# Kernel optimization log

Hardware: AMD Instinct MI355X
Metric: run time of the kernel (lower is better)

Reference implementation:

```python
import jax, jax.numpy as jnp
import numpy as np

N_NODES = 50000
N_EDGES = 800000
IN_DIM, HID_DIM, OUT_DIM = 128, 256, 40


def setup_inputs() -> dict:
    key = jax.random.key(0)
    ks = jax.random.split(key, 8)
    x = jax.random.normal(ks[0], (N_NODES, IN_DIM), dtype=jnp.float32)
    edge_index = jax.random.randint(ks[1], (2, N_EDGES), 0, N_NODES, dtype=jnp.int64)
    s1 = 1.0 / np.sqrt(IN_DIM)
    s2 = 1.0 / np.sqrt(HID_DIM)
    return {
        "x": x,
        "edge_index": edge_index,
        "W1_l": jax.random.normal(ks[2], (IN_DIM, HID_DIM), dtype=jnp.float32) * s1,
        "W1_r": jax.random.normal(ks[3], (IN_DIM, HID_DIM), dtype=jnp.float32) * s1,
        "b1": jnp.zeros((HID_DIM,), dtype=jnp.float32),
        "W2_l": jax.random.normal(ks[4], (HID_DIM, OUT_DIM), dtype=jnp.float32) * s2,
        "W2_r": jax.random.normal(ks[5], (HID_DIM, OUT_DIM), dtype=jnp.float32) * s2,
        "b2": jnp.zeros((OUT_DIM,), dtype=jnp.float32),
    }


def _sage_conv(x, src, dst, W_l, W_r, b, n_nodes):
    # mean aggregation of source features onto destination nodes
    agg = jax.ops.segment_sum(x[src], dst, num_segments=n_nodes)  # [N, d]
    cnt = jax.ops.segment_sum(jnp.ones(src.shape[0], x.dtype), dst, num_segments=n_nodes)
    agg = agg / jnp.maximum(cnt, 1.0)[:, None]
    # PyG SAGEConv: lin_l(aggr) + lin_r(x), bias in lin_l
    return agg @ W_l + x @ W_r + b


def reference(x, edge_index, W1_l, W1_r, b1, W2_l, W2_r, b2):
    src, dst = edge_index[0], edge_index[1]
    n = x.shape[0]
    h = jax.nn.relu(_sage_conv(x, src, dst, W1_l, W1_r, b1, n))
    # dropout is identity in eval mode
    out = _sage_conv(h, src, dst, W2_l, W2_r, b2, n)
    return jax.nn.log_softmax(out, axis=1)
```

## Files before the change

### kernel.cpp

```cpp
#include <hip/hip_runtime.h>
#include <hip/hip_bf16.h>

#define N_NODES 50000
#define N_EDGES 800000
#define IN_DIM 128
#define HID_DIM 256
#define OUT_DIM 40
#define M_PAD 50048
#define NBUCKETS 782
#define EPB 8192
#define BINA_BLOCKS 98
#define BLK_PAD 128

#define OFF_RP     0
#define OFF_ESRC   200064
#define OFF_STAGE  3400064
#define OFF_HISTG  6600064
#define OFF_PFXG   7000448
#define OFF_BTOT   7400832
#define OFF_BBASE  7403968
#define OFF_AB     7407104
#define OFF_H      33031680
#define OFF_W1T    58656256
#define OFF_W2T    58787328
#define OFF_P2     58828288
#define OFF_R2     62832128

typedef __attribute__((ext_vector_type(8))) short short8;
typedef __attribute__((ext_vector_type(4))) float f32x4;

__device__ __forceinline__ float bfu2f(unsigned u) {
  union { unsigned i; float f; } c; c.i = u << 16; return c.f;
}
__device__ __forceinline__ unsigned f2bfu(float f) {
  union { float f; unsigned i; } c; c.f = f;
  return (c.i + 0x7fffu + ((c.i >> 16) & 1u)) >> 16;
}

#define GLOAD_LDS16(g, l)                                                      \
  __builtin_amdgcn_global_load_lds(                                            \
      (const __attribute__((address_space(1))) void*)(g),                      \
      (__attribute__((address_space(3))) void*)(l), 16, 0, 0)

__global__ __launch_bounds__(1024) void k_hist(const int* __restrict__ dst,
                                               int* __restrict__ hist_g) {
  __shared__ int hist[NBUCKETS];
  int t = threadIdx.x, blk = blockIdx.x;
  for (int b = t; b < NBUCKETS; b += 1024) hist[b] = 0;
  __syncthreads();
  int e0 = blk * EPB, e1 = min(e0 + EPB, N_EDGES);
  for (int e = e0 + t; e < e1; e += 1024) atomicAdd(&hist[dst[e] >> 6], 1);
  __syncthreads();
  for (int b = t; b < NBUCKETS; b += 1024) hist_g[b * BLK_PAD + blk] = hist[b];
}

__global__ __launch_bounds__(256) void k_hscanA(const int* __restrict__ hist_g,
                                                int* __restrict__ pfx_g,
                                                int* __restrict__ btot) {
  int wave = blockIdx.x * 4 + (threadIdx.x >> 6);
  int lane = threadIdx.x & 63;
  if (wave >= NBUCKETS) return;
  const int* h = hist_g + wave * BLK_PAD;
  int v0 = (lane < BINA_BLOCKS) ? h[lane] : 0;
  int v1 = (lane + 64 < BINA_BLOCKS) ? h[lane + 64] : 0;
  int s0 = v0;
#pragma unroll
  for (int d = 1; d < 64; d <<= 1) {
    int u = __shfl_up(s0, d, 64);
    if (lane >= d) s0 += u;
  }
  int tot0 = __shfl(s0, 63, 64);
  int s1 = v1;
#pragma unroll
  for (int d = 1; d < 64; d <<= 1) {
    int u = __shfl_up(s1, d, 64);
    if (lane >= d) s1 += u;
  }
  s1 += tot0;
  pfx_g[wave * BLK_PAD + lane] = s0 - v0;
  if (lane + 64 < BLK_PAD) pfx_g[wave * BLK_PAD + lane + 64] = s1 - v1;
  if (lane == 63) btot[wave] = s1;
}

__global__ __launch_bounds__(1024) void k_hscanB(const int* __restrict__ btot,
                                                 int* __restrict__ bbase,
                                                 int* __restrict__ row_ptr) {
  __shared__ int part[1024];
  int t = threadIdx.x;
  int v = (t < NBUCKETS) ? btot[t] : 0;
  part[t] = v;
  __syncthreads();
  for (int off = 1; off < 1024; off <<= 1) {
    int u = (t >= off) ? part[t - off] : 0;
    __syncthreads();
    part[t] += u;
    __syncthreads();
  }
  if (t < NBUCKETS) bbase[t] = part[t] - v;
  if (t == NBUCKETS - 1) {
    bbase[NBUCKETS] = part[t];
    row_ptr[N_NODES] = part[t];
  }
}

__global__ __launch_bounds__(1024) void k_fill2(const int* __restrict__ src,
                                                const int* __restrict__ dst,
                                                const int* __restrict__ bbase,
                                                const int* __restrict__ pfx_g,
                                                unsigned* __restrict__ stage) {
  __shared__ int cur[NBUCKETS];
  int t = threadIdx.x, blk = blockIdx.x;
  for (int b = t; b < NBUCKETS; b += 1024)
    cur[b] = bbase[b] + pfx_g[b * BLK_PAD + blk];
  __syncthreads();
  int e0 = blk * EPB, e1 = min(e0 + EPB, N_EDGES);
  for (int e = e0 + t; e < e1; e += 1024) {
    int d = dst[e];
    int pos = atomicAdd(&cur[d >> 6], 1);
    stage[pos] = ((unsigned)src[e] << 6) | (unsigned)(d & 63);
  }
}

__global__ __launch_bounds__(256) void k_bsort(const unsigned* __restrict__ stage,
                                               const int* __restrict__ bbase,
                                               int* __restrict__ row_ptr,
                                               int* __restrict__ esrc) {
  __shared__ int lcnt[64];
  __shared__ int lout[1536];
  int b = blockIdx.x, t = threadIdx.x;
  int base = bbase[b];
  int nb = bbase[b + 1] - base;
  if (t < 64) lcnt[t] = 0;
  __syncthreads();
  const unsigned* sp = stage + base;
  for (int e = t; e < nb; e += 256) atomicAdd(&lcnt[sp[e] & 63u], 1);
  __syncthreads();
  if (t < 64) {
    int v = lcnt[t];
    int s = v;
#pragma unroll
    for (int d = 1; d < 64; d <<= 1) {
      int u = __shfl_up(s, d, 64);
      if (t >= d) s += u;
    }
    int node = b * 64 + t;
    if (node < N_NODES) row_ptr[node] = base + s - v;
    lcnt[t] = s - v;
  }
  __syncthreads();
  for (int e = t; e < nb; e += 256) {
    unsigned p = sp[e];
    int lp = atomicAdd(&lcnt[p & 63u], 1);
    lout[lp] = (int)(p >> 6);
  }
  __syncthreads();
  for (int i = t; i < nb; i += 256) esrc[base + i] = lout[i];
}

__global__ __launch_bounds__(256) void k_convx(const float* __restrict__ x,
                                               char* __restrict__ ABb) {
  int t = blockIdx.x * 256 + threadIdx.x;
  int row = t >> 4, c8 = (t & 15) << 3;
  if (row >= N_NODES) return;
  const float* xp = x + (size_t)row * IN_DIM + c8;
  unsigned short o[8];
#pragma unroll
  for (int i = 0; i < 8; ++i) o[i] = (unsigned short)f2bfu(xp[i]);
  *(short8*)(ABb + (size_t)row * 512 + 256 + c8 * 2) = *(short8*)o;
}

__global__ __launch_bounds__(256) void k_convw(const float* __restrict__ W1l,
                                               const float* __restrict__ W1r,
                                               const float* __restrict__ W2l,
                                               const float* __restrict__ W2r,
                                               unsigned short* __restrict__ Wt1,
                                               unsigned short* __restrict__ Wt2) {
  int k = threadIdx.x;
  if (blockIdx.x < 256) {
    int n = blockIdx.x;
    float v = (k < 128) ? W1l[(size_t)k * HID_DIM + n]
                        : W1r[(size_t)(k - 128) * HID_DIM + n];
    Wt1[(size_t)n * 256 + k] = (unsigned short)f2bfu(v);
  } else {
    int n = blockIdx.x - 256;
    float v = (n < OUT_DIM) ? W2l[(size_t)k * OUT_DIM + n]
                            : W2r[(size_t)k * OUT_DIM + (n - OUT_DIM)];
    Wt2[(size_t)n * 256 + k] = (unsigned short)f2bfu(v);
  }
}

__global__ __launch_bounds__(256) void k_agg1(char* __restrict__ ABb,
    const int* __restrict__ row_ptr, const int* __restrict__ esrc) {
  int tid = threadIdx.x;
  int node = blockIdx.x * 4 + (tid >> 6);
  int lane = tid & 63;
  int g = lane >> 4;
  int q = lane & 15;
  int beg = row_ptr[node], end = row_ptr[node + 1];
  float s[8];
#pragma unroll
  for (int j = 0; j < 8; ++j) s[j] = 0.f;

  for (int e0 = beg; e0 < end; e0 += 4) {
    int e = e0 + g;
    if (e < end) {
      int srcn = esrc[e];
      short8 v = *(const short8*)(ABb + (size_t)srcn * 512 + 256 + q * 16);
#pragma unroll
      for (int j = 0; j < 8; ++j)
        s[j] += bfu2f((unsigned short)v[j]);
    }
  }
#pragma unroll
  for (int j = 0; j < 8; ++j) {
    s[j] += __shfl_xor(s[j], 16, 64);
    s[j] += __shfl_xor(s[j], 32, 64);
  }
  float inv = 1.0f / (float)max(end - beg, 1);
  if (lane < 16) {
    unsigned short o[8];
#pragma unroll
    for (int j = 0; j < 8; ++j) o[j] = (unsigned short)f2bfu(s[j] * inv);
    *(short8*)(ABb + (size_t)node * 512 + q * 16) = *(short8*)o;
  }
}

__global__ __launch_bounds__(256) void k_gemm1(
    const char* __restrict__ ABb, const short* __restrict__ Wt1,
    const float* __restrict__ b1, unsigned short* __restrict__ H) {
  __shared__ __align__(16) char As[64 * 512];
  const int tid = threadIdx.x;
  const int w = tid >> 6, lane = tid & 63;
  const int row0 = blockIdx.x * 64;

  {
    const char* gbase = ABb + (size_t)row0 * 512;
#pragma unroll
    for (int i = 0; i < 8; ++i) {
      int o = i * 4096 + w * 1024 + lane * 16;
      int row = o >> 9;
      int kslot = ((o & 511) >> 4) ^ (row & 7);
      GLOAD_LDS16(gbase + row * 512 + kslot * 16, As + i * 4096 + w * 1024);
    }
  }
  __syncthreads();

  f32x4 acc[4][4];
#pragma unroll
  for (int mi = 0; mi < 4; ++mi)
#pragma unroll
    for (int ni = 0; ni < 4; ++ni) acc[mi][ni] = (f32x4){0.f, 0.f, 0.f, 0.f};

  const short* wb = Wt1 + (size_t)(w * 64 + (lane & 15)) * 256 + (lane >> 4) * 8;

  for (int ks = 0; ks < 8; ++ks) {
    short8 af[4], bf[4];
#pragma unroll
    for (int mi = 0; mi < 4; ++mi) {
      int row = mi * 16 + (lane & 15);
      int kslot = (ks * 4 + (lane >> 4)) ^ (row & 7);
      af[mi] = *(const short8*)(As + row * 512 + kslot * 16);
    }
#pragma unroll
    for (int ni = 0; ni < 4; ++ni)
      bf[ni] = *(const short8*)(wb + ni * 16 * 256 + ks * 32);
#pragma unroll
    for (int mi = 0; mi < 4; ++mi)
#pragma unroll
      for (int ni = 0; ni < 4; ++ni)
        acc[mi][ni] = __builtin_amdgcn_mfma_f32_16x16x32_bf16(
            af[mi], bf[ni], acc[mi][ni], 0, 0, 0);
  }

#pragma unroll
  for (int ni = 0; ni < 4; ++ni) {
    int col = w * 64 + ni * 16 + (lane & 15);
    float bv = b1[col];
#pragma unroll
    for (int mi = 0; mi < 4; ++mi) {
      int rbase = row0 + mi * 16 + (lane >> 4) * 4;
#pragma unroll
      for (int r = 0; r < 4; ++r) {
        float v = fmaxf(acc[mi][ni][r] + bv, 0.f);
        H[(size_t)(rbase + r) * 256 + col] = (unsigned short)f2bfu(v);
      }
    }
  }
}

__global__ __launch_bounds__(256) void k_gemm2(
    const char* __restrict__ Hb, const short* __restrict__ Wt2,
    const float* __restrict__ b2, unsigned short* __restrict__ P2,
    float* __restrict__ R2) {
  __shared__ __align__(16) char As[64 * 512];
  const int tid = threadIdx.x;
  const int w = tid >> 6, lane = tid & 63;
  const int row0 = blockIdx.x * 64;

  {
    const char* gbase = Hb + (size_t)row0 * 512;
#pragma unroll
    for (int i = 0; i < 8; ++i) {
      int o = i * 4096 + w * 1024 + lane * 16;
      int row = o >> 9;
      int kslot = ((o & 511) >> 4) ^ (row & 7);
      GLOAD_LDS16(gbase + row * 512 + kslot * 16, As + i * 4096 + w * 1024);
    }
  }
  __syncthreads();

  f32x4 acc[5];
#pragma unroll
  for (int ni = 0; ni < 5; ++ni) acc[ni] = (f32x4){0.f, 0.f, 0.f, 0.f};

  const short* wb = Wt2 + (size_t)(lane & 15) * 256 + (lane >> 4) * 8;
  const int arow = w * 16 + (lane & 15);

  for (int ks = 0; ks < 8; ++ks) {
    int kslot = (ks * 4 + (lane >> 4)) ^ (arow & 7);
    short8 a = *(const short8*)(As + arow * 512 + kslot * 16);
#pragma unroll
    for (int ni = 0; ni < 5; ++ni) {
      short8 bf = *(const short8*)(wb + ni * 16 * 256 + ks * 32);
      acc[ni] = __builtin_amdgcn_mfma_f32_16x16x32_bf16(a, bf, acc[ni], 0, 0, 0);
    }
  }

#pragma unroll
  for (int ni = 0; ni < 5; ++ni) {
    int col = ni * 16 + (lane & 15);
#pragma unroll
    for (int r = 0; r < 4; ++r) {
      int row = row0 + w * 16 + (lane >> 4) * 4 + r;
      float v = acc[ni][r];
      if (col < OUT_DIM) {
        P2[(size_t)row * OUT_DIM + col] = (unsigned short)f2bfu(v);
      } else {
        R2[(size_t)row * OUT_DIM + (col - OUT_DIM)] = v + b2[col - OUT_DIM];
      }
    }
  }
}

__global__ __launch_bounds__(256) void k_agg2(const unsigned short* __restrict__ P2,
    const float* __restrict__ R2, const int* __restrict__ row_ptr,
    const int* __restrict__ esrc, float* __restrict__ out) {
  int tid = threadIdx.x;
  int node = blockIdx.x * 4 + (tid >> 6);
  int lane = tid & 63;
  int g = lane >> 3;
  int q = lane & 7;
  int beg = row_ptr[node], end = row_ptr[node + 1];
  float s[8];
#pragma unroll
  for (int j = 0; j < 8; ++j) s[j] = 0.f;

  for (int e0 = beg; e0 < end; e0 += 8) {
    int e = e0 + g;
    if (e < end && q < 5) {
      int srcn = esrc[e];
      short8 v = *(const short8*)((const char*)P2 + (size_t)srcn * 80 + q * 16);
#pragma unroll
      for (int j = 0; j < 8; ++j)
        s[j] += bfu2f((unsigned short)v[j]);
    }
  }
#pragma unroll
  for (int j = 0; j < 8; ++j) {
    s[j] += __shfl_xor(s[j], 8, 64);
    s[j] += __shfl_xor(s[j], 16, 64);
    s[j] += __shfl_xor(s[j], 32, 64);
  }

  float inv = 1.0f / (float)max(end - beg, 1);
  float v[8];
  float m = -1e30f;
  if (q < 5) {
    const float* rr = R2 + (size_t)node * OUT_DIM + q * 8;
    f32x4 r0 = *(const f32x4*)rr;
    f32x4 r1 = *(const f32x4*)(rr + 4);
#pragma unroll
    for (int j = 0; j < 8; ++j) {
      float rj = (j < 4) ? r0[j] : r1[j - 4];
      v[j] = s[j] * inv + rj;
      m = fmaxf(m, v[j]);
    }
  }
#pragma unroll
  for (int o = 1; o <= 4; o <<= 1) m = fmaxf(m, __shfl_xor(m, o, 64));
  float ex = 0.f;
  if (q < 5) {
#pragma unroll
    for (int j = 0; j < 8; ++j) ex += __expf(v[j] - m);
  }
#pragma unroll
  for (int o = 1; o <= 4; o <<= 1) ex += __shfl_xor(ex, o, 64);
  float ls = __logf(ex) + m;

  if (g == 0 && q < 5) {
    float* op = out + (size_t)node * OUT_DIM + q * 8;
    f32x4 o0, o1;
#pragma unroll
    for (int j = 0; j < 4; ++j) { o0[j] = v[j] - ls; o1[j] = v[j + 4] - ls; }
    *(f32x4*)op = o0;
    *(f32x4*)(op + 4) = o1;
  }
}

extern "C" void kernel_launch(void* const* d_in, const int* in_sizes, int n_in,
                              void* d_out, int out_size, void* d_ws, size_t ws_size,
                              hipStream_t stream) {
  const float* x   = (const float*)d_in[0];
  const int*   ei  = (const int*)d_in[1];
  const float* W1l = (const float*)d_in[2];
  const float* W1r = (const float*)d_in[3];
  const float* b1  = (const float*)d_in[4];
  const float* W2l = (const float*)d_in[5];
  const float* W2r = (const float*)d_in[6];
  const float* b2  = (const float*)d_in[7];
  float* out = (float*)d_out;

  const int* src = ei;
  const int* dst = ei + N_EDGES;

  char* ws = (char*)d_ws;
  int*      row_ptr = (int*)(ws + OFF_RP);
  int*      esrc    = (int*)(ws + OFF_ESRC);
  unsigned* stage   = (unsigned*)(ws + OFF_STAGE);
  int*      hist_g  = (int*)(ws + OFF_HISTG);
  int*      pfx_g   = (int*)(ws + OFF_PFXG);
  int*      btot    = (int*)(ws + OFF_BTOT);
  int*      bbase   = (int*)(ws + OFF_BBASE);
  char*     ABb     = ws + OFF_AB;
  char*     Hb      = ws + OFF_H;
  unsigned short* Wt1 = (unsigned short*)(ws + OFF_W1T);
  unsigned short* Wt2 = (unsigned short*)(ws + OFF_W2T);
  unsigned short* P2  = (unsigned short*)(ws + OFF_P2);
  float* R2 = (float*)(ws + OFF_R2);

  (void)hipMemsetAsync(ABb + (size_t)N_NODES * 512, 0, (M_PAD - N_NODES) * 512,
                       stream);

  k_convx<<<(N_NODES * 16 + 255) / 256, 256, 0, stream>>>(x, ABb);
  k_convw<<<336, 256, 0, stream>>>(W1l, W1r, W2l, W2r, Wt1, Wt2);

  k_hist<<<BINA_BLOCKS, 1024, 0, stream>>>(dst, hist_g);
  k_hscanA<<<(NBUCKETS + 3) / 4, 256, 0, stream>>>(hist_g, pfx_g, btot);
  k_hscanB<<<1, 1024, 0, stream>>>(btot, bbase, row_ptr);
  k_fill2<<<BINA_BLOCKS, 1024, 0, stream>>>(src, dst, bbase, pfx_g, stage);
  k_bsort<<<NBUCKETS, 256, 0, stream>>>(stage, bbase, row_ptr, esrc);

  k_agg1<<<N_NODES / 4, 256, 0, stream>>>(ABb, row_ptr, esrc);
  k_gemm1<<<M_PAD / 64, 256, 0, stream>>>(ABb, (const short*)Wt1, b1,
                                          (unsigned short*)Hb);
  k_gemm2<<<M_PAD / 64, 256, 0, stream>>>(Hb, (const short*)Wt2, b2, P2, R2);
  k_agg2<<<N_NODES / 4, 256, 0, stream>>>(P2, R2, row_ptr, esrc, out);
}
```

Measured before the change: 229.0 us.

## Fuse two GEMMs through LDS, merge conversion kernels, unroll agg1 gathers

The layer-1 GEMM and the layer-2 projection GEMM now run in one kernel. The ReLU'd hidden tile is written as bf16 into the swizzled LDS buffer and consumed directly by the second MFMA loop, so the 25MB H intermediate no longer makes a round trip through global memory. The x and weight conversion kernels are merged into a single launch. agg1 now issues two neighbor gathers per iteration with clamped indices and zero weights, which raises memory-level parallelism at the cost of some redundant loads on the tail.

```diff
diff --git a/kernel.cpp b/kernel.cpp
--- a/kernel.cpp
+++ b/kernel.cpp
@@ -11,6 +11,7 @@
 #define EPB 8192
 #define BINA_BLOCKS 98
 #define BLK_PAD 128
+#define CONVX_BLOCKS 3125
 
 #define OFF_RP     0
 #define OFF_ESRC   200064
@@ -20,11 +21,10 @@
 #define OFF_BTOT   7400832
 #define OFF_BBASE  7403968
 #define OFF_AB     7407104
-#define OFF_H      33031680
-#define OFF_W1T    58656256
-#define OFF_W2T    58787328
-#define OFF_P2     58828288
-#define OFF_R2     62832128
+#define OFF_W1T    33031680
+#define OFF_W2T    33162752
+#define OFF_P2     33203712
+#define OFF_R2     37207552
 
 typedef __attribute__((ext_vector_type(8))) short short8;
 typedef __attribute__((ext_vector_type(4))) float f32x4;
@@ -157,32 +157,31 @@
   for (int i = t; i < nb; i += 256) esrc[base + i] = lout[i];
 }
 
-__global__ __launch_bounds__(256) void k_convx(const float* __restrict__ x,
-                                               char* __restrict__ ABb) {
-  int t = blockIdx.x * 256 + threadIdx.x;
-  int row = t >> 4, c8 = (t & 15) << 3;
-  if (row >= N_NODES) return;
-  const float* xp = x + (size_t)row * IN_DIM + c8;
-  unsigned short o[8];
-#pragma unroll
-  for (int i = 0; i < 8; ++i) o[i] = (unsigned short)f2bfu(xp[i]);
-  *(short8*)(ABb + (size_t)row * 512 + 256 + c8 * 2) = *(short8*)o;
-}
-
-__global__ __launch_bounds__(256) void k_convw(const float* __restrict__ W1l,
-                                               const float* __restrict__ W1r,
-                                               const float* __restrict__ W2l,
-                                               const float* __restrict__ W2r,
-                                               unsigned short* __restrict__ Wt1,
-                                               unsigned short* __restrict__ Wt2) {
-  int k = threadIdx.x;
-  if (blockIdx.x < 256) {
-    int n = blockIdx.x;
+__global__ __launch_bounds__(256) void k_conv(const float* __restrict__ x,
+                                              char* __restrict__ ABb,
+                                              const float* __restrict__ W1l,
+                                              const float* __restrict__ W1r,
+                                              const float* __restrict__ W2l,
+                                              const float* __restrict__ W2r,
+                                              unsigned short* __restrict__ Wt1,
+                                              unsigned short* __restrict__ Wt2) {
+  if (blockIdx.x < CONVX_BLOCKS) {
+    int t = blockIdx.x * 256 + threadIdx.x;
+    int row = t >> 4, c8 = (t & 15) << 3;
+    const float* xp = x + (size_t)row * IN_DIM + c8;
+    unsigned short o[8];
+#pragma unroll
+    for (int i = 0; i < 8; ++i) o[i] = (unsigned short)f2bfu(xp[i]);
+    *(short8*)(ABb + (size_t)row * 512 + 256 + c8 * 2) = *(short8*)o;
+  } else if (blockIdx.x < CONVX_BLOCKS + 256) {
+    int n = blockIdx.x - CONVX_BLOCKS;
+    int k = threadIdx.x;
     float v = (k < 128) ? W1l[(size_t)k * HID_DIM + n]
                         : W1r[(size_t)(k - 128) * HID_DIM + n];
     Wt1[(size_t)n * 256 + k] = (unsigned short)f2bfu(v);
   } else {
-    int n = blockIdx.x - 256;
+    int n = blockIdx.x - CONVX_BLOCKS - 256;
+    int k = threadIdx.x;
     float v = (n < OUT_DIM) ? W2l[(size_t)k * OUT_DIM + n]
                             : W2r[(size_t)k * OUT_DIM + (n - OUT_DIM)];
     Wt2[(size_t)n * 256 + k] = (unsigned short)f2bfu(v);
@@ -201,15 +200,22 @@
 #pragma unroll
   for (int j = 0; j < 8; ++j) s[j] = 0.f;
 
-  for (int e0 = beg; e0 < end; e0 += 4) {
-    int e = e0 + g;
-    if (e < end) {
-      int srcn = esrc[e];
-      short8 v = *(const short8*)(ABb + (size_t)srcn * 512 + 256 + q * 16);
-#pragma unroll
-      for (int j = 0; j < 8; ++j)
-        s[j] += bfu2f((unsigned short)v[j]);
-    }
+  for (int e0 = beg; e0 < end; e0 += 8) {
+    int eA = e0 + g;
+    int eB = eA + 4;
+    int iA = min(eA, end - 1);
+    int iB = min(eB, end - 1);
+    int sA = esrc[iA], sB = esrc[iB];
+    float wA = (eA < end) ? 1.f : 0.f;
+    float wB = (eB < end) ? 1.f : 0.f;
+    short8 vA = *(const short8*)(ABb + (size_t)sA * 512 + 256 + q * 16);
+    short8 vB = *(const short8*)(ABb + (size_t)sB * 512 + 256 + q * 16);
+#pragma unroll
+    for (int j = 0; j < 8; ++j)
+      s[j] = fmaf(wA, bfu2f((unsigned short)vA[j]), s[j]);
+#pragma unroll
+    for (int j = 0; j < 8; ++j)
+      s[j] = fmaf(wB, bfu2f((unsigned short)vB[j]), s[j]);
   }
 #pragma unroll
   for (int j = 0; j < 8; ++j) {
@@ -225,71 +231,9 @@
   }
 }
 
-__global__ __launch_bounds__(256) void k_gemm1(
+__global__ __launch_bounds__(256) void k_gemm(
     const char* __restrict__ ABb, const short* __restrict__ Wt1,
-    const float* __restrict__ b1, unsigned short* __restrict__ H) {
-  __shared__ __align__(16) char As[64 * 512];
-  const int tid = threadIdx.x;
-  const int w = tid >> 6, lane = tid & 63;
-  const int row0 = blockIdx.x * 64;
-
-  {
-    const char* gbase = ABb + (size_t)row0 * 512;
-#pragma unroll
-    for (int i = 0; i < 8; ++i) {
-      int o = i * 4096 + w * 1024 + lane * 16;
-      int row = o >> 9;
-      int kslot = ((o & 511) >> 4) ^ (row & 7);
-      GLOAD_LDS16(gbase + row * 512 + kslot * 16, As + i * 4096 + w * 1024);
-    }
-  }
-  __syncthreads();
-
-  f32x4 acc[4][4];
-#pragma unroll
-  for (int mi = 0; mi < 4; ++mi)
-#pragma unroll
-    for (int ni = 0; ni < 4; ++ni) acc[mi][ni] = (f32x4){0.f, 0.f, 0.f, 0.f};
-
-  const short* wb = Wt1 + (size_t)(w * 64 + (lane & 15)) * 256 + (lane >> 4) * 8;
-
-  for (int ks = 0; ks < 8; ++ks) {
-    short8 af[4], bf[4];
-#pragma unroll
-    for (int mi = 0; mi < 4; ++mi) {
-      int row = mi * 16 + (lane & 15);
-      int kslot = (ks * 4 + (lane >> 4)) ^ (row & 7);
-      af[mi] = *(const short8*)(As + row * 512 + kslot * 16);
-    }
-#pragma unroll
-    for (int ni = 0; ni < 4; ++ni)
-      bf[ni] = *(const short8*)(wb + ni * 16 * 256 + ks * 32);
-#pragma unroll
-    for (int mi = 0; mi < 4; ++mi)
-#pragma unroll
-      for (int ni = 0; ni < 4; ++ni)
-        acc[mi][ni] = __builtin_amdgcn_mfma_f32_16x16x32_bf16(
-            af[mi], bf[ni], acc[mi][ni], 0, 0, 0);
-  }
-
-#pragma unroll
-  for (int ni = 0; ni < 4; ++ni) {
-    int col = w * 64 + ni * 16 + (lane & 15);
-    float bv = b1[col];
-#pragma unroll
-    for (int mi = 0; mi < 4; ++mi) {
-      int rbase = row0 + mi * 16 + (lane >> 4) * 4;
-#pragma unroll
-      for (int r = 0; r < 4; ++r) {
-        float v = fmaxf(acc[mi][ni][r] + bv, 0.f);
-        H[(size_t)(rbase + r) * 256 + col] = (unsigned short)f2bfu(v);
-      }
-    }
-  }
-}
-
-__global__ __launch_bounds__(256) void k_gemm2(
-    const char* __restrict__ Hb, const short* __restrict__ Wt2,
+    const short* __restrict__ Wt2, const float* __restrict__ b1,
     const float* __restrict__ b2, unsigned short* __restrict__ P2,
     float* __restrict__ R2) {
   __shared__ __align__(16) char As[64 * 512];
@@ -298,7 +242,7 @@
   const int row0 = blockIdx.x * 64;
 
   {
-    const char* gbase = Hb + (size_t)row0 * 512;
+    const char* gbase = ABb + (size_t)row0 * 512;
 #pragma unroll
     for (int i = 0; i < 8; ++i) {
       int o = i * 4096 + w * 1024 + lane * 16;
@@ -309,11 +253,58 @@
   }
   __syncthreads();
 
-  f32x4 acc[5];
-#pragma unroll
-  for (int ni = 0; ni < 5; ++ni) acc[ni] = (f32x4){0.f, 0.f, 0.f, 0.f};
-
-  const short* wb = Wt2 + (size_t)(lane & 15) * 256 + (lane >> 4) * 8;
+  f32x4 acc[4][4];
+#pragma unroll
+  for (int mi = 0; mi < 4; ++mi)
+#pragma unroll
+    for (int ni = 0; ni < 4; ++ni) acc[mi][ni] = (f32x4){0.f, 0.f, 0.f, 0.f};
+
+  const short* wb1 = Wt1 + (size_t)(w * 64 + (lane & 15)) * 256 + (lane >> 4) * 8;
+
+  for (int ks = 0; ks < 8; ++ks) {
+    short8 af[4], bf[4];
+#pragma unroll
+    for (int mi = 0; mi < 4; ++mi) {
+      int row = mi * 16 + (lane & 15);
+      int kslot = (ks * 4 + (lane >> 4)) ^ (row & 7);
+      af[mi] = *(const short8*)(As + row * 512 + kslot * 16);
+    }
+#pragma unroll
+    for (int ni = 0; ni < 4; ++ni)
+      bf[ni] = *(const short8*)(wb1 + ni * 16 * 256 + ks * 32);
+#pragma unroll
+    for (int mi = 0; mi < 4; ++mi)
+#pragma unroll
+      for (int ni = 0; ni < 4; ++ni)
+        acc[mi][ni] = __builtin_amdgcn_mfma_f32_16x16x32_bf16(
+            af[mi], bf[ni], acc[mi][ni], 0, 0, 0);
+  }
+
+  __syncthreads();
+
+#pragma unroll
+  for (int ni = 0; ni < 4; ++ni) {
+    int col = w * 64 + ni * 16 + (lane & 15);
+    float bv = b1[col];
+#pragma unroll
+    for (int mi = 0; mi < 4; ++mi) {
+#pragma unroll
+      for (int r = 0; r < 4; ++r) {
+        int row = mi * 16 + (lane >> 4) * 4 + r;
+        float v = fmaxf(acc[mi][ni][r] + bv, 0.f);
+        int gr = (col >> 3) ^ (row & 7);
+        *(unsigned short*)(As + row * 512 + gr * 16 + (col & 7) * 2) =
+            (unsigned short)f2bfu(v);
+      }
+    }
+  }
+  __syncthreads();
+
+  f32x4 acc2[5];
+#pragma unroll
+  for (int ni = 0; ni < 5; ++ni) acc2[ni] = (f32x4){0.f, 0.f, 0.f, 0.f};
+
+  const short* wb2 = Wt2 + (size_t)(lane & 15) * 256 + (lane >> 4) * 8;
   const int arow = w * 16 + (lane & 15);
 
   for (int ks = 0; ks < 8; ++ks) {
@@ -321,8 +312,8 @@
     short8 a = *(const short8*)(As + arow * 512 + kslot * 16);
 #pragma unroll
     for (int ni = 0; ni < 5; ++ni) {
-      short8 bf = *(const short8*)(wb + ni * 16 * 256 + ks * 32);
-      acc[ni] = __builtin_amdgcn_mfma_f32_16x16x32_bf16(a, bf, acc[ni], 0, 0, 0);
+      short8 bf = *(const short8*)(wb2 + ni * 16 * 256 + ks * 32);
+      acc2[ni] = __builtin_amdgcn_mfma_f32_16x16x32_bf16(a, bf, acc2[ni], 0, 0, 0);
     }
   }
 
@@ -332,7 +323,7 @@
 #pragma unroll
     for (int r = 0; r < 4; ++r) {
       int row = row0 + w * 16 + (lane >> 4) * 4 + r;
-      float v = acc[ni][r];
+      float v = acc2[ni][r];
       if (col < OUT_DIM) {
         P2[(size_t)row * OUT_DIM + col] = (unsigned short)f2bfu(v);
       } else {
@@ -432,7 +423,6 @@
   int*      btot    = (int*)(ws + OFF_BTOT);
   int*      bbase   = (int*)(ws + OFF_BBASE);
   char*     ABb     = ws + OFF_AB;
-  char*     Hb      = ws + OFF_H;
   unsigned short* Wt1 = (unsigned short*)(ws + OFF_W1T);
   unsigned short* Wt2 = (unsigned short*)(ws + OFF_W2T);
   unsigned short* P2  = (unsigned short*)(ws + OFF_P2);
@@ -441,8 +431,8 @@
   (void)hipMemsetAsync(ABb + (size_t)N_NODES * 512, 0, (M_PAD - N_NODES) * 512,
                        stream);
 
-  k_convx<<<(N_NODES * 16 + 255) / 256, 256, 0, stream>>>(x, ABb);
-  k_convw<<<336, 256, 0, stream>>>(W1l, W1r, W2l, W2r, Wt1, Wt2);
+  k_conv<<<CONVX_BLOCKS + 336, 256, 0, stream>>>(x, ABb, W1l, W1r, W2l, W2r,
+                                                 Wt1, Wt2);
 
   k_hist<<<BINA_BLOCKS, 1024, 0, stream>>>(dst, hist_g);
   k_hscanA<<<(NBUCKETS + 3) / 4, 256, 0, stream>>>(hist_g, pfx_g, btot);
@@ -451,8 +441,7 @@
   k_bsort<<<NBUCKETS, 256, 0, stream>>>(stage, bbase, row_ptr, esrc);
 
   k_agg1<<<N_NODES / 4, 256, 0, stream>>>(ABb, row_ptr, esrc);
-  k_gemm1<<<M_PAD / 64, 256, 0, stream>>>(ABb, (const short*)Wt1, b1,
-                                          (unsigned short*)Hb);
-  k_gemm2<<<M_PAD / 64, 256, 0, stream>>>(Hb, (const short*)Wt2, b2, P2, R2);
+  k_gemm<<<M_PAD / 64, 256, 0, stream>>>(ABb, (const short*)Wt1,
+                                         (const short*)Wt2, b1, b2, P2, R2);
   k_agg2<<<N_NODES / 4, 256, 0, stream>>>(P2, R2, row_ptr, esrc, out);
 }
```

After: 212.0 us. 1.08x faster.
